# Kernel optimization log

Hardware: AMD Instinct MI355X
Metric: run time of the kernel (lower is better)

Reference implementation:

```python
import jax, jax.numpy as jnp
import numpy as np

N, M, E = 400000, 100000, 3200000
C_FEAT = 61            # per-point feature channels
D_IN = 64              # 3 (rel xyz) + C_FEAT
D0, D1, D2 = 64, 128, 256  # mlp = [64, 128, 256]
EPS = 1e-5


def setup_inputs() -> dict:
    key = jax.random.key(0)
    ks = jax.random.split(key, 16)
    inp = {}
    inp['point_bxyz'] = jax.random.uniform(ks[0], (N, 4), dtype=jnp.float32) * 50.0
    inp['point_feat'] = jax.random.normal(ks[1], (N, C_FEAT), dtype=jnp.float32)
    inp['sample_idx'] = jax.random.randint(ks[2], (M,), 0, N)
    inp['e_point'] = jax.random.randint(ks[3], (E,), 0, N)
    inp['e_new'] = jnp.sort(jax.random.randint(ks[4], (E,), 0, M))
    # PointConv: Linear(D_IN -> D0)
    inp['W0'] = jax.random.normal(ks[5], (D_IN, D0), dtype=jnp.float32) / np.sqrt(D_IN)
    inp['b0'] = jnp.zeros((D0,), dtype=jnp.float32)
    # mlp_convs[0]: Linear(D0 -> D1) + BN
    inp['W1'] = jax.random.normal(ks[6], (D0, D1), dtype=jnp.float32) / np.sqrt(D0)
    inp['b1'] = jnp.zeros((D1,), dtype=jnp.float32)
    inp['g1'] = jnp.ones((D1,), dtype=jnp.float32)
    inp['beta1'] = jnp.zeros((D1,), dtype=jnp.float32)
    # mlp_convs[1]: Linear(D1 -> D2) + BN
    inp['W2'] = jax.random.normal(ks[7], (D1, D2), dtype=jnp.float32) / np.sqrt(D1)
    inp['b2'] = jnp.zeros((D2,), dtype=jnp.float32)
    inp['g2'] = jnp.ones((D2,), dtype=jnp.float32)
    inp['beta2'] = jnp.zeros((D2,), dtype=jnp.float32)
    return inp


def _bn_relu(x, g, b):
    # BatchNorm1d in training mode: batch stats, biased variance
    mu = x.mean(axis=0)
    var = x.var(axis=0)
    return jax.nn.relu((x - mu) * jax.lax.rsqrt(var + EPS) * g + b)


def reference(point_bxyz, point_feat, sample_idx, e_point, e_new,
              W0, b0, W1, b1, g1, beta1, W2, b2, g2, beta2):
    num_new = sample_idx.shape[0]
    new_bxyz = point_bxyz[sample_idx]                      # [M, 4]
    # PointConv: per-edge relative position encoding + feature gather
    rel = point_bxyz[e_point, 1:4] - new_bxyz[e_new, 1:4]  # [E, 3]
    edge_in = jnp.concatenate([rel, point_feat[e_point]], axis=-1)  # [E, D_IN]
    h = jax.nn.relu(edge_in @ W0 + b0)                     # [E, D0]
    # per-neighborhood max aggregation (scatter-max), empty segments -> 0
    agg = jax.ops.segment_max(h, e_new, num_segments=num_new)
    agg = jnp.where(jnp.isneginf(agg), 0.0, agg)           # [M, D0]
    # trailing Linear + BN + ReLU stack
    x = _bn_relu(agg @ W1 + b1, g1, beta1)                 # [M, D1]
    x = _bn_relu(x @ W2 + b2, g2, beta2)                   # [M, D2]
    return new_bxyz, x
```

## Files before the change

### kernel.cpp

```cpp
#include <hip/hip_runtime.h>

#define EPS 1e-5f
#define ECHUNK 64
#define PF 8

typedef _Float16 half8 __attribute__((ext_vector_type(8)));
typedef _Float16 half4v __attribute__((ext_vector_type(4)));
typedef float float4v __attribute__((ext_vector_type(4)));

__global__ void gather_kernel(const float4* __restrict__ bxyz, const int* __restrict__ sidx,
                              float4* __restrict__ out, int M) {
    int i = blockIdx.x * blockDim.x + threadIdx.x;
    if (i < M) out[i] = bxyz[sidx[i]];
}

__global__ void w2t_kernel(const float* __restrict__ W2, _Float16* __restrict__ W2h) {
    int i = blockIdx.x * blockDim.x + threadIdx.x;
    int n = i & 255, k = i >> 8;
    W2h[(size_t)n * 128 + k] = (_Float16)W2[(size_t)k * 256 + n];
}

__global__ __launch_bounds__(256, 4) void point_kernel(
    const float* __restrict__ feat, const float4* __restrict__ bxyz4,
    const float* __restrict__ W0, const float* __restrict__ b0,
    _Float16* __restrict__ GDh, int N) {
    __shared__ float Xt[64 * 68];
    __shared__ float Ws[64 * 64];
    __shared__ float w0s[192];
    int t = threadIdx.x;
    int row0 = blockIdx.x * 64;
    for (int i = t; i < 64 * 61; i += 256) {
        int r = i / 61, k = i - r * 61;
        int rr = min(row0 + r, N - 1);
        Xt[k * 68 + r] = feat[(size_t)rr * 61 + k];
    }
    for (int i = t; i < 61 * 64; i += 256) {
        int k = i >> 6, c = i & 63;
        Ws[i] = W0[(size_t)(3 + k) * 64 + c];
    }
    if (t < 192) { int k = 61 + t / 64, j = t % 64; Xt[k * 68 + j] = 0.f; Ws[k * 64 + j] = 0.f; w0s[t] = W0[t]; }
    __syncthreads();
    int c0 = (t & 15) * 4;
    int r0 = (t >> 4) * 4;
    float acc[4][4] = {};
#pragma unroll 4
    for (int k = 0; k < 64; ++k) {
        float4 x = *(const float4*)&Xt[k * 68 + r0];
        float4 w = *(const float4*)&Ws[k * 64 + c0];
        float xv[4] = {x.x, x.y, x.z, x.w};
        float wv[4] = {w.x, w.y, w.z, w.w};
#pragma unroll
        for (int rr = 0; rr < 4; ++rr)
#pragma unroll
            for (int cc = 0; cc < 4; ++cc)
                acc[rr][cc] = fmaf(xv[rr], wv[cc], acc[rr][cc]);
    }
    float4 bb = *(const float4*)&b0[c0];
    float bv[4] = {bb.x, bb.y, bb.z, bb.w};
    float wx[4], wy[4], wz[4];
#pragma unroll
    for (int cc = 0; cc < 4; ++cc) {
        wx[cc] = w0s[c0 + cc];
        wy[cc] = w0s[64 + c0 + cc];
        wz[cc] = w0s[128 + c0 + cc];
    }
#pragma unroll
    for (int rr = 0; rr < 4; ++rr) {
        int r = row0 + r0 + rr;
        if (r < N) {
            float4 P = bxyz4[r];
            half4v o;
#pragma unroll
            for (int cc = 0; cc < 4; ++cc) {
                float d = fmaf(P.y, wx[cc], fmaf(P.z, wy[cc], P.w * wz[cc]));
                o[cc] = (_Float16)(acc[rr][cc] + bv[cc] + d);
            }
            *(half4v*)&GDh[(size_t)r * 64 + c0] = o;
        }
    }
}

__global__ __launch_bounds__(256, 4) void edge_kernel(
    const float4* __restrict__ nbxyz4,
    const int* __restrict__ e_point, const int* __restrict__ e_new,
    const _Float16* __restrict__ GDh, const float* __restrict__ W0,
    float* __restrict__ agg, int E) {
    int lane = threadIdx.x & 63;
    int gwave = blockIdx.x * 4 + (threadIdx.x >> 6);
    int base = gwave * ECHUNK;
    if (base >= E) return;
    int n = min(ECHUNK, E - base);
    int idx = min(base + lane, E - 1);
    int ep = e_point[idx];
    int en = e_new[idx];
    float wx = W0[lane], wy = W0[64 + lane], wz = W0[128 + lane];
    float runmax = 0.f;
    int curseg = -1;
    float S = 0.f;
    for (int g0 = 0; g0 < n; g0 += PF) {
        _Float16 gu[PF];
#pragma unroll
        for (int j = 0; j < PF; ++j) {
            int p = __builtin_amdgcn_readlane(ep, g0 + j);
            gu[j] = GDh[(size_t)p * 64 + lane];
        }
#pragma unroll
        for (int j = 0; j < PF; ++j) {
            if (g0 + j >= n) break;
            int s = __builtin_amdgcn_readlane(en, g0 + j);
            if (s != curseg) {
                if (curseg >= 0)
                    atomicMax((int*)&agg[(size_t)curseg * 64 + lane], __float_as_int(runmax));
                curseg = s;
                runmax = 0.f;
                float4 Q = nbxyz4[s];
                S = fmaf(Q.y, wx, fmaf(Q.z, wy, Q.w * wz));
            }
            float h = (float)gu[j] - S;
            runmax = fmaxf(runmax, h);
        }
    }
    if (curseg >= 0)
        atomicMax((int*)&agg[(size_t)curseg * 64 + lane], __float_as_int(runmax));
}

__global__ __launch_bounds__(256, 4) void gemm1_kernel(
    const float* __restrict__ agg, const float* __restrict__ W1,
    float* __restrict__ y1, float* __restrict__ p1sum, float* __restrict__ p1sq, int M) {
    __shared__ float Xt[64 * 68];
    __shared__ float Ws[64 * 128];
    float* red = Xt;
    int t = threadIdx.x;
    int row0 = blockIdx.x * 64;
#pragma unroll
    for (int j = 0; j < 4; ++j) {
        int idx4 = t + j * 256;
        int r = idx4 >> 4, k4 = idx4 & 15;
        float4 v = make_float4(0.f, 0.f, 0.f, 0.f);
        if (row0 + r < M) v = ((const float4*)agg)[(size_t)(row0 + r) * 16 + k4];
        Xt[(k4 * 4 + 0) * 68 + r] = v.x;
        Xt[(k4 * 4 + 1) * 68 + r] = v.y;
        Xt[(k4 * 4 + 2) * 68 + r] = v.z;
        Xt[(k4 * 4 + 3) * 68 + r] = v.w;
    }
#pragma unroll
    for (int j = 0; j < 8; ++j) {
        int idx4 = t + j * 256;
        ((float4*)Ws)[idx4] = ((const float4*)W1)[idx4];
    }
    __syncthreads();
    int c0 = (t & 15) * 8;
    int r0 = (t >> 4) * 4;
    float acc[4][8] = {};
#pragma unroll 4
    for (int k = 0; k < 64; ++k) {
        float4 x = *(const float4*)&Xt[k * 68 + r0];
        float4 wa = *(const float4*)&Ws[k * 128 + c0];
        float4 wb = *(const float4*)&Ws[k * 128 + c0 + 4];
        float xv[4] = {x.x, x.y, x.z, x.w};
        float wv[8] = {wa.x, wa.y, wa.z, wa.w, wb.x, wb.y, wb.z, wb.w};
#pragma unroll
        for (int rr = 0; rr < 4; ++rr)
#pragma unroll
            for (int cc = 0; cc < 8; ++cc)
                acc[rr][cc] = fmaf(xv[rr], wv[cc], acc[rr][cc]);
    }
    float s[8] = {}, q[8] = {};
#pragma unroll
    for (int rr = 0; rr < 4; ++rr) {
        int r = row0 + r0 + rr;
        if (r < M) {
            *(float4*)&y1[(size_t)r * 128 + c0] = make_float4(acc[rr][0], acc[rr][1], acc[rr][2], acc[rr][3]);
            *(float4*)&y1[(size_t)r * 128 + c0 + 4] = make_float4(acc[rr][4], acc[rr][5], acc[rr][6], acc[rr][7]);
        }
#pragma unroll
        for (int cc = 0; cc < 8; ++cc) { float a = acc[rr][cc]; s[cc] += a; q[cc] += a * a; }
    }
    __syncthreads();
    int colg = t & 15, rowg = t >> 4;
#pragma unroll
    for (int cc = 0; cc < 8; ++cc) {
        int c = colg * 8 + cc;
        red[c * 17 + rowg] = s[cc];
        red[2176 + c * 17 + rowg] = q[cc];
    }
    __syncthreads();
    if (t < 128) {
        float ss = 0.f, qq = 0.f;
#pragma unroll
        for (int i = 0; i < 16; ++i) { ss += red[t * 17 + i]; qq += red[2176 + t * 17 + i]; }
        p1sum[(size_t)blockIdx.x * 128 + t] = ss;
        p1sq[(size_t)blockIdx.x * 128 + t] = qq;
    }
}

__global__ void stats_kernel(const float* __restrict__ psum, const float* __restrict__ psq,
                             const float* __restrict__ g, const float* __restrict__ beta,
                             float* __restrict__ scale, float* __restrict__ shift,
                             int nblk, int ncols, float invM) {
    __shared__ float ss[256], qq[256];
    int c = blockIdx.x;
    int t = threadIdx.x;
    float s = 0.f, q = 0.f;
    for (int b = t; b < nblk; b += 256) {
        s += psum[(size_t)b * ncols + c];
        q += psq[(size_t)b * ncols + c];
    }
    ss[t] = s; qq[t] = q;
    __syncthreads();
    for (int off = 128; off > 0; off >>= 1) {
        if (t < off) { ss[t] += ss[t + off]; qq[t] += qq[t + off]; }
        __syncthreads();
    }
    if (t == 0) {
        float mean = ss[0] * invM;
        float var = qq[0] * invM - mean * mean;
        float sc = g[c] * rsqrtf(var + EPS);
        scale[c] = sc;
        shift[c] = beta[c] - mean * sc;
    }
}

__global__ __launch_bounds__(256, 2) void gemm2_kernel(
    const float* __restrict__ y1, const _Float16* __restrict__ W2h,
    const float* __restrict__ scale1, const float* __restrict__ shift1,
    float* __restrict__ yout, float* __restrict__ p2sum, float* __restrict__ p2sq,
    int M, int nbn) {
    __shared__ _Float16 As[128 * 136];
    __shared__ _Float16 Bs[128 * 136];
    int t = threadIdx.x;
    int bm = blockIdx.x / nbn;
    int bn = blockIdx.x % nbn;
    int row0 = bm * 128;
#pragma unroll
    for (int j = 0; j < 16; ++j) {
        int idx4 = t + j * 256;
        int r = idx4 >> 5, k4 = idx4 & 31;
        float4 v = make_float4(0.f, 0.f, 0.f, 0.f);
        if (row0 + r < M) {
            float4 y = ((const float4*)y1)[(size_t)(row0 + r) * 32 + k4];
            float4 sc = ((const float4*)scale1)[k4];
            float4 sh = ((const float4*)shift1)[k4];
            v.x = fmaxf(0.f, fmaf(y.x, sc.x, sh.x));
            v.y = fmaxf(0.f, fmaf(y.y, sc.y, sh.y));
            v.z = fmaxf(0.f, fmaf(y.z, sc.z, sh.z));
            v.w = fmaxf(0.f, fmaf(y.w, sc.w, sh.w));
        }
        half4v h;
        h[0] = (_Float16)v.x; h[1] = (_Float16)v.y; h[2] = (_Float16)v.z; h[3] = (_Float16)v.w;
        *(half4v*)&As[r * 136 + k4 * 4] = h;
    }
    int n0 = bn * 128;
#pragma unroll
    for (int j = 0; j < 8; ++j) {
        int idx8 = t + j * 256;
        int nn = idx8 >> 4, k8 = idx8 & 15;
        *(half8*)&Bs[nn * 136 + k8 * 8] = *(const half8*)&W2h[(size_t)(n0 + nn) * 128 + k8 * 8];
    }
    __syncthreads();
    int w = t >> 6, lane = t & 63;
    int quad = lane >> 4, l16 = lane & 15;
    int mwave = (w >> 1) * 64, nwave = (w & 1) * 64;
    float4v acc[4][4] = {};
#pragma unroll
    for (int kc = 0; kc < 4; ++kc) {
        int koff = kc * 32 + quad * 8;
        half8 af[4], bf[4];
#pragma unroll
        for (int mt = 0; mt < 4; ++mt)
            af[mt] = *(const half8*)&As[(mwave + mt * 16 + l16) * 136 + koff];
#pragma unroll
        for (int nt = 0; nt < 4; ++nt)
            bf[nt] = *(const half8*)&Bs[(nwave + nt * 16 + l16) * 136 + koff];
#pragma unroll
        for (int mt = 0; mt < 4; ++mt)
#pragma unroll
            for (int nt = 0; nt < 4; ++nt)
                acc[mt][nt] = __builtin_amdgcn_mfma_f32_16x16x32_f16(af[mt], bf[nt], acc[mt][nt], 0, 0, 0);
    }
    float s[4] = {}, q[4] = {};
    int colbase = n0 + nwave + l16;
#pragma unroll
    for (int mt = 0; mt < 4; ++mt) {
#pragma unroll
        for (int i = 0; i < 4; ++i) {
            int row = row0 + mwave + mt * 16 + quad * 4 + i;
            if (row < M) {
#pragma unroll
                for (int nt = 0; nt < 4; ++nt)
                    yout[(size_t)row * 256 + colbase + nt * 16] = acc[mt][nt][i];
            }
#pragma unroll
            for (int nt = 0; nt < 4; ++nt) {
                float a = acc[mt][nt][i];
                s[nt] += a; q[nt] += a * a;
            }
        }
    }
    __syncthreads();
    float* red = (float*)As;
    int slot = (w >> 1) * 4 + quad;
#pragma unroll
    for (int nt = 0; nt < 4; ++nt) {
        int c = (w & 1) * 64 + nt * 16 + l16;
        red[c * 8 + slot] = s[nt];
        red[1024 + c * 8 + slot] = q[nt];
    }
    __syncthreads();
    if (t < 128) {
        float ss = 0.f, qq = 0.f;
#pragma unroll
        for (int i = 0; i < 8; ++i) { ss += red[t * 8 + i]; qq += red[1024 + t * 8 + i]; }
        p2sum[(size_t)bm * 256 + n0 + t] = ss;
        p2sq[(size_t)bm * 256 + n0 + t] = qq;
    }
}

__global__ void apply2_kernel(float4* __restrict__ x, const float* __restrict__ scale2,
                              const float* __restrict__ shift2, int n4) {
    int i = blockIdx.x * blockDim.x + threadIdx.x;
    if (i >= n4) return;
    int c4 = i & 63;
    float4 v = x[i];
    float4 sc = ((const float4*)scale2)[c4];
    float4 sh = ((const float4*)shift2)[c4];
    v.x = fmaxf(0.f, fmaf(v.x, sc.x, sh.x));
    v.y = fmaxf(0.f, fmaf(v.y, sc.y, sh.y));
    v.z = fmaxf(0.f, fmaf(v.z, sc.z, sh.z));
    v.w = fmaxf(0.f, fmaf(v.w, sc.w, sh.w));
    x[i] = v;
}

extern "C" void kernel_launch(void* const* d_in, const int* in_sizes, int n_in,
                              void* d_out, int out_size, void* d_ws, size_t ws_size,
                              hipStream_t stream) {
    const float* bxyz  = (const float*)d_in[0];
    const float* feat  = (const float*)d_in[1];
    const int*   sidx  = (const int*)d_in[2];
    const int*   e_point = (const int*)d_in[3];
    const int*   e_new = (const int*)d_in[4];
    const float* W0    = (const float*)d_in[5];
    const float* b0    = (const float*)d_in[6];
    const float* W1    = (const float*)d_in[7];
    const float* g1    = (const float*)d_in[9];
    const float* beta1 = (const float*)d_in[10];
    const float* W2    = (const float*)d_in[11];
    const float* g2    = (const float*)d_in[13];
    const float* beta2 = (const float*)d_in[14];
    int N = in_sizes[0] / 4;
    int M = in_sizes[2];
    int E = in_sizes[3];

    float* out0 = (float*)d_out;
    float* out1 = (float*)d_out + (size_t)M * 4;

    float* ws = (float*)d_ws;
    size_t o = 0;
    float* agg = ws + o; o += (size_t)M * 64;
    float* y1  = ws + o; o += (size_t)M * 128;
    _Float16* GDh = (_Float16*)(ws + o); o += (size_t)N * 32;
    _Float16* W2h = (_Float16*)(ws + o); o += 128 * 256 / 2;
    int nblk1 = (M + 63) / 64;
    int nblk2m = (M + 127) / 128;
    int nbn = 2;
    float* p1sum = ws + o; o += (size_t)nblk1 * 128;
    float* p1sq  = ws + o; o += (size_t)nblk1 * 128;
    float* p2sum = ws + o; o += (size_t)nblk2m * 256;
    float* p2sq  = ws + o; o += (size_t)nblk2m * 256;
    float* scale1 = ws + o; o += 128;
    float* shift1 = ws + o; o += 128;
    float* scale2 = ws + o; o += 256;
    float* shift2 = ws + o; o += 256;

    hipMemsetAsync(agg, 0, (size_t)M * 64 * sizeof(float), stream);
    gather_kernel<<<(M + 255) / 256, 256, 0, stream>>>((const float4*)bxyz, sidx, (float4*)out0, M);
    w2t_kernel<<<128, 256, 0, stream>>>(W2, W2h);
    point_kernel<<<(N + 63) / 64, 256, 0, stream>>>(feat, (const float4*)bxyz, W0, b0, GDh, N);
    int nwaves = (E + ECHUNK - 1) / ECHUNK;
    edge_kernel<<<(nwaves + 3) / 4, 256, 0, stream>>>((const float4*)out0, e_point, e_new,
                                                      GDh, W0, agg, E);
    gemm1_kernel<<<nblk1, 256, 0, stream>>>(agg, W1, y1, p1sum, p1sq, M);
    stats_kernel<<<128, 256, 0, stream>>>(p1sum, p1sq, g1, beta1, scale1, shift1, nblk1, 128, 1.f / M);
    gemm2_kernel<<<nblk2m * nbn, 256, 0, stream>>>(y1, W2h, scale1, shift1, out1, p2sum, p2sq, M, nbn);
    stats_kernel<<<256, 256, 0, stream>>>(p2sum, p2sq, g2, beta2, scale2, shift2, nblk2m, 256, 1.f / M);
    apply2_kernel<<<((M * 64) + 255) / 256, 256, 0, stream>>>((float4*)out1, scale2, shift2, M * 64);
}
```

Baseline: 463.7 us.

## Move point and gemm1 GEMMs to fp16 MFMA and store y1 in fp16

Rewrites point_kernel and gemm1_kernel to use fp16 MFMA 16x16x32 instructions with 128-row tiles in place of scalar fp32 FMA loops. A single prep kernel now converts and transposes W0, W1 and W2 to fp16. The intermediate y1 is stored as fp16 to halve its traffic between gemm1 and gemm2. Point xyz is now folded into the GEMM input (fp16) rather than added in fp32, which lowers precision of the per-point features and the BN statistics inputs.

Result: faster. 404.8 us (-12.7%).

```diff
diff --git a/kernel.cpp b/kernel.cpp
--- a/kernel.cpp
+++ b/kernel.cpp
@@ -14,69 +14,93 @@
     if (i < M) out[i] = bxyz[sidx[i]];
 }
 
-__global__ void w2t_kernel(const float* __restrict__ W2, _Float16* __restrict__ W2h) {
+__global__ void prep_kernel(const float* __restrict__ W0, const float* __restrict__ W1,
+                            const float* __restrict__ W2, _Float16* __restrict__ W0t,
+                            _Float16* __restrict__ W1t, _Float16* __restrict__ W2t) {
     int i = blockIdx.x * blockDim.x + threadIdx.x;
-    int n = i & 255, k = i >> 8;
-    W2h[(size_t)n * 128 + k] = (_Float16)W2[(size_t)k * 256 + n];
+    if (i < 4096) {
+        int k = i >> 6, n = i & 63;
+        W0t[(size_t)n * 64 + k] = (_Float16)W0[i];
+    } else if (i < 12288) {
+        int j = i - 4096; int k = j >> 7, n = j & 127;
+        W1t[(size_t)n * 64 + k] = (_Float16)W1[j];
+    } else if (i < 45056) {
+        int j = i - 12288; int k = j >> 8, n = j & 255;
+        W2t[(size_t)n * 128 + k] = (_Float16)W2[j];
+    }
 }
 
 __global__ __launch_bounds__(256, 4) void point_kernel(
     const float* __restrict__ feat, const float4* __restrict__ bxyz4,
-    const float* __restrict__ W0, const float* __restrict__ b0,
+    const _Float16* __restrict__ W0t, const float* __restrict__ b0,
     _Float16* __restrict__ GDh, int N) {
-    __shared__ float Xt[64 * 68];
-    __shared__ float Ws[64 * 64];
-    __shared__ float w0s[192];
+    __shared__ _Float16 As[128 * 72];
     int t = threadIdx.x;
-    int row0 = blockIdx.x * 64;
-    for (int i = t; i < 64 * 61; i += 256) {
-        int r = i / 61, k = i - r * 61;
-        int rr = min(row0 + r, N - 1);
-        Xt[k * 68 + r] = feat[(size_t)rr * 61 + k];
-    }
-    for (int i = t; i < 61 * 64; i += 256) {
-        int k = i >> 6, c = i & 63;
-        Ws[i] = W0[(size_t)(3 + k) * 64 + c];
-    }
-    if (t < 192) { int k = 61 + t / 64, j = t % 64; Xt[k * 68 + j] = 0.f; Ws[k * 64 + j] = 0.f; w0s[t] = W0[t]; }
-    __syncthreads();
-    int c0 = (t & 15) * 4;
-    int r0 = (t >> 4) * 4;
-    float acc[4][4] = {};
-#pragma unroll 4
-    for (int k = 0; k < 64; ++k) {
-        float4 x = *(const float4*)&Xt[k * 68 + r0];
-        float4 w = *(const float4*)&Ws[k * 64 + c0];
-        float xv[4] = {x.x, x.y, x.z, x.w};
-        float wv[4] = {w.x, w.y, w.z, w.w};
-#pragma unroll
-        for (int rr = 0; rr < 4; ++rr)
-#pragma unroll
-            for (int cc = 0; cc < 4; ++cc)
-                acc[rr][cc] = fmaf(xv[rr], wv[cc], acc[rr][cc]);
-    }
-    float4 bb = *(const float4*)&b0[c0];
-    float bv[4] = {bb.x, bb.y, bb.z, bb.w};
-    float wx[4], wy[4], wz[4];
-#pragma unroll
-    for (int cc = 0; cc < 4; ++cc) {
-        wx[cc] = w0s[c0 + cc];
-        wy[cc] = w0s[64 + c0 + cc];
-        wz[cc] = w0s[128 + c0 + cc];
-    }
-#pragma unroll
-    for (int rr = 0; rr < 4; ++rr) {
-        int r = row0 + r0 + rr;
-        if (r < N) {
-            float4 P = bxyz4[r];
-            half4v o;
-#pragma unroll
-            for (int cc = 0; cc < 4; ++cc) {
-                float d = fmaf(P.y, wx[cc], fmaf(P.z, wy[cc], P.w * wz[cc]));
-                o[cc] = (_Float16)(acc[rr][cc] + bv[cc] + d);
-            }
-            *(half4v*)&GDh[(size_t)r * 64 + c0] = o;
-        }
+    int row0 = blockIdx.x * 128;
+    if (t < 128) {
+        int r = min(row0 + t, N - 1);
+        float4 P = bxyz4[r];
+        As[t * 72 + 0] = (_Float16)P.y;
+        As[t * 72 + 1] = (_Float16)P.z;
+        As[t * 72 + 2] = (_Float16)P.w;
+    }
+    const float* fbase = feat + (size_t)row0 * 61;
+    int avail = (int)min((size_t)7808, (size_t)(N - row0) * 61);
+#pragma unroll
+    for (int j = 0; j < 8; ++j) {
+        int base = (t + j * 256) * 4;
+        if (base < avail) {
+            float4 v = *(const float4*)&fbase[base];
+            float fv[4] = {v.x, v.y, v.z, v.w};
+#pragma unroll
+            for (int u = 0; u < 4; ++u) {
+                int flat = base + u;
+                int r = flat / 61;
+                int k = flat - r * 61;
+                As[r * 72 + 3 + k] = (_Float16)fv[u];
+            }
+        }
+    }
+    __syncthreads();
+    int w = t >> 6, lane = t & 63, quad = lane >> 4, l16 = lane & 15;
+    int mwave = w * 32;
+    float4v acc[2][4] = {};
+#pragma unroll
+    for (int kc = 0; kc < 2; ++kc) {
+        int koff = kc * 32 + quad * 8;
+        half8 af[2], bf[4];
+#pragma unroll
+        for (int mt = 0; mt < 2; ++mt)
+            af[mt] = *(const half8*)&As[(mwave + mt * 16 + l16) * 72 + koff];
+#pragma unroll
+        for (int nt = 0; nt < 4; ++nt)
+            bf[nt] = *(const half8*)&W0t[(size_t)(nt * 16 + l16) * 64 + koff];
+#pragma unroll
+        for (int mt = 0; mt < 2; ++mt)
+#pragma unroll
+            for (int nt = 0; nt < 4; ++nt)
+                acc[mt][nt] = __builtin_amdgcn_mfma_f32_16x16x32_f16(af[mt], bf[nt], acc[mt][nt], 0, 0, 0);
+    }
+    float b0v[4];
+#pragma unroll
+    for (int nt = 0; nt < 4; ++nt) b0v[nt] = b0[nt * 16 + l16];
+    __syncthreads();
+#pragma unroll
+    for (int mt = 0; mt < 2; ++mt)
+#pragma unroll
+        for (int i = 0; i < 4; ++i) {
+            int rloc = mwave + mt * 16 + quad * 4 + i;
+#pragma unroll
+            for (int nt = 0; nt < 4; ++nt)
+                As[rloc * 72 + nt * 16 + l16] = (_Float16)(acc[mt][nt][i] + b0v[nt]);
+        }
+    __syncthreads();
+#pragma unroll
+    for (int j = 0; j < 4; ++j) {
+        int i8 = t + j * 256;
+        int r = i8 >> 3, c8 = i8 & 7;
+        if (row0 + r < N)
+            *(half8*)&GDh[(size_t)(row0 + r) * 64 + c8 * 8] = *(const half8*)&As[r * 72 + c8 * 8];
     }
 }
 
@@ -124,73 +148,89 @@
         atomicMax((int*)&agg[(size_t)curseg * 64 + lane], __float_as_int(runmax));
 }
 
-__global__ __launch_bounds__(256, 4) void gemm1_kernel(
-    const float* __restrict__ agg, const float* __restrict__ W1,
-    float* __restrict__ y1, float* __restrict__ p1sum, float* __restrict__ p1sq, int M) {
-    __shared__ float Xt[64 * 68];
-    __shared__ float Ws[64 * 128];
-    float* red = Xt;
+__global__ __launch_bounds__(256, 2) void gemm1_kernel(
+    const float* __restrict__ agg, const _Float16* __restrict__ W1t,
+    _Float16* __restrict__ y1h, float* __restrict__ p1sum, float* __restrict__ p1sq, int M) {
+    __shared__ _Float16 As[128 * 72];
+    __shared__ float red[4096];
     int t = threadIdx.x;
-    int row0 = blockIdx.x * 64;
-#pragma unroll
-    for (int j = 0; j < 4; ++j) {
-        int idx4 = t + j * 256;
-        int r = idx4 >> 4, k4 = idx4 & 15;
+    int row0 = blockIdx.x * 128;
+#pragma unroll
+    for (int j = 0; j < 8; ++j) {
+        int i4 = t + j * 256;
+        int r = i4 >> 4, k4 = i4 & 15;
         float4 v = make_float4(0.f, 0.f, 0.f, 0.f);
         if (row0 + r < M) v = ((const float4*)agg)[(size_t)(row0 + r) * 16 + k4];
-        Xt[(k4 * 4 + 0) * 68 + r] = v.x;
-        Xt[(k4 * 4 + 1) * 68 + r] = v.y;
-        Xt[(k4 * 4 + 2) * 68 + r] = v.z;
-        Xt[(k4 * 4 + 3) * 68 + r] = v.w;
-    }
-#pragma unroll
-    for (int j = 0; j < 8; ++j) {
-        int idx4 = t + j * 256;
-        ((float4*)Ws)[idx4] = ((const float4*)W1)[idx4];
-    }
-    __syncthreads();
-    int c0 = (t & 15) * 8;
-    int r0 = (t >> 4) * 4;
-    float acc[4][8] = {};
-#pragma unroll 4
-    for (int k = 0; k < 64; ++k) {
-        float4 x = *(const float4*)&Xt[k * 68 + r0];
-        float4 wa = *(const float4*)&Ws[k * 128 + c0];
-        float4 wb = *(const float4*)&Ws[k * 128 + c0 + 4];
-        float xv[4] = {x.x, x.y, x.z, x.w};
-        float wv[8] = {wa.x, wa.y, wa.z, wa.w, wb.x, wb.y, wb.z, wb.w};
-#pragma unroll
-        for (int rr = 0; rr < 4; ++rr)
-#pragma unroll
-            for (int cc = 0; cc < 8; ++cc)
-                acc[rr][cc] = fmaf(xv[rr], wv[cc], acc[rr][cc]);
+        half4v h;
+        h[0] = (_Float16)v.x; h[1] = (_Float16)v.y; h[2] = (_Float16)v.z; h[3] = (_Float16)v.w;
+        *(half4v*)&As[r * 72 + k4 * 4] = h;
+    }
+    __syncthreads();
+    int w = t >> 6, lane = t & 63, quad = lane >> 4, l16 = lane & 15;
+    int mwave = w * 32;
+    float4v acc[2][8] = {};
+#pragma unroll
+    for (int kc = 0; kc < 2; ++kc) {
+        int koff = kc * 32 + quad * 8;
+        half8 af[2], bf[8];
+#pragma unroll
+        for (int mt = 0; mt < 2; ++mt)
+            af[mt] = *(const half8*)&As[(mwave + mt * 16 + l16) * 72 + koff];
+#pragma unroll
+        for (int nt = 0; nt < 8; ++nt)
+            bf[nt] = *(const half8*)&W1t[(size_t)(nt * 16 + l16) * 64 + koff];
+#pragma unroll
+        for (int mt = 0; mt < 2; ++mt)
+#pragma unroll
+            for (int nt = 0; nt < 8; ++nt)
+                acc[mt][nt] = __builtin_amdgcn_mfma_f32_16x16x32_f16(af[mt], bf[nt], acc[mt][nt], 0, 0, 0);
     }
     float s[8] = {}, q[8] = {};
 #pragma unroll
-    for (int rr = 0; rr < 4; ++rr) {
-        int r = row0 + r0 + rr;
-        if (r < M) {
-            *(float4*)&y1[(size_t)r * 128 + c0] = make_float4(acc[rr][0], acc[rr][1], acc[rr][2], acc[rr][3]);
-            *(float4*)&y1[(size_t)r * 128 + c0 + 4] = make_float4(acc[rr][4], acc[rr][5], acc[rr][6], acc[rr][7]);
-        }
-#pragma unroll
-        for (int cc = 0; cc < 8; ++cc) { float a = acc[rr][cc]; s[cc] += a; q[cc] += a * a; }
-    }
-    __syncthreads();
-    int colg = t & 15, rowg = t >> 4;
-#pragma unroll
-    for (int cc = 0; cc < 8; ++cc) {
-        int c = colg * 8 + cc;
-        red[c * 17 + rowg] = s[cc];
-        red[2176 + c * 17 + rowg] = q[cc];
+    for (int mt = 0; mt < 2; ++mt)
+#pragma unroll
+        for (int i = 0; i < 4; ++i)
+#pragma unroll
+            for (int nt = 0; nt < 8; ++nt) {
+                float a = acc[mt][nt][i];
+                s[nt] += a; q[nt] += a * a;
+            }
+    int slot = w * 4 + quad;
+#pragma unroll
+    for (int nt = 0; nt < 8; ++nt) {
+        int c = nt * 16 + l16;
+        red[c * 16 + slot] = s[nt];
+        red[2048 + c * 16 + slot] = q[nt];
     }
     __syncthreads();
     if (t < 128) {
         float ss = 0.f, qq = 0.f;
 #pragma unroll
-        for (int i = 0; i < 16; ++i) { ss += red[t * 17 + i]; qq += red[2176 + t * 17 + i]; }
+        for (int i = 0; i < 16; ++i) { ss += red[t * 16 + i]; qq += red[2048 + t * 16 + i]; }
         p1sum[(size_t)blockIdx.x * 128 + t] = ss;
         p1sq[(size_t)blockIdx.x * 128 + t] = qq;
+    }
+#pragma unroll
+    for (int half = 0; half < 2; ++half) {
+#pragma unroll
+        for (int mt = 0; mt < 2; ++mt)
+#pragma unroll
+            for (int i = 0; i < 4; ++i) {
+                int rloc = mwave + mt * 16 + quad * 4 + i;
+#pragma unroll
+                for (int nt = 0; nt < 4; ++nt)
+                    As[rloc * 72 + nt * 16 + l16] = (_Float16)acc[mt][half * 4 + nt][i];
+            }
+        __syncthreads();
+#pragma unroll
+        for (int j = 0; j < 4; ++j) {
+            int i8 = t + j * 256;
+            int r = i8 >> 3, c8 = i8 & 7;
+            if (row0 + r < M)
+                *(half8*)&y1h[(size_t)(row0 + r) * 128 + half * 64 + c8 * 8] =
+                    *(const half8*)&As[r * 72 + c8 * 8];
+        }
+        __syncthreads();
     }
 }
 
@@ -222,7 +262,7 @@
 }
 
 __global__ __launch_bounds__(256, 2) void gemm2_kernel(
-    const float* __restrict__ y1, const _Float16* __restrict__ W2h,
+    const _Float16* __restrict__ y1h, const _Float16* __restrict__ W2t,
     const float* __restrict__ scale1, const float* __restrict__ shift1,
     float* __restrict__ yout, float* __restrict__ p2sum, float* __restrict__ p2sq,
     int M, int nbn) {
@@ -233,29 +273,30 @@
     int bn = blockIdx.x % nbn;
     int row0 = bm * 128;
 #pragma unroll
-    for (int j = 0; j < 16; ++j) {
-        int idx4 = t + j * 256;
-        int r = idx4 >> 5, k4 = idx4 & 31;
-        float4 v = make_float4(0.f, 0.f, 0.f, 0.f);
+    for (int j = 0; j < 8; ++j) {
+        int i8 = t + j * 256;
+        int r = i8 >> 4, k8 = i8 & 15;
+        half8 hv = {};
         if (row0 + r < M) {
-            float4 y = ((const float4*)y1)[(size_t)(row0 + r) * 32 + k4];
-            float4 sc = ((const float4*)scale1)[k4];
-            float4 sh = ((const float4*)shift1)[k4];
-            v.x = fmaxf(0.f, fmaf(y.x, sc.x, sh.x));
-            v.y = fmaxf(0.f, fmaf(y.y, sc.y, sh.y));
-            v.z = fmaxf(0.f, fmaf(y.z, sc.z, sh.z));
-            v.w = fmaxf(0.f, fmaf(y.w, sc.w, sh.w));
-        }
-        half4v h;
-        h[0] = (_Float16)v.x; h[1] = (_Float16)v.y; h[2] = (_Float16)v.z; h[3] = (_Float16)v.w;
-        *(half4v*)&As[r * 136 + k4 * 4] = h;
+            half8 y = *(const half8*)&y1h[(size_t)(row0 + r) * 128 + k8 * 8];
+            float4 sca = ((const float4*)scale1)[k8 * 2];
+            float4 scb = ((const float4*)scale1)[k8 * 2 + 1];
+            float4 sha = ((const float4*)shift1)[k8 * 2];
+            float4 shb = ((const float4*)shift1)[k8 * 2 + 1];
+            float sc[8] = {sca.x, sca.y, sca.z, sca.w, scb.x, scb.y, scb.z, scb.w};
+            float sh[8] = {sha.x, sha.y, sha.z, sha.w, shb.x, shb.y, shb.z, shb.w};
+#pragma unroll
+            for (int u = 0; u < 8; ++u)
+                hv[u] = (_Float16)fmaxf(0.f, fmaf((float)y[u], sc[u], sh[u]));
+        }
+        *(half8*)&As[r * 136 + k8 * 8] = hv;
     }
     int n0 = bn * 128;
 #pragma unroll
     for (int j = 0; j < 8; ++j) {
-        int idx8 = t + j * 256;
-        int nn = idx8 >> 4, k8 = idx8 & 15;
-        *(half8*)&Bs[nn * 136 + k8 * 8] = *(const half8*)&W2h[(size_t)(n0 + nn) * 128 + k8 * 8];
+        int i8 = t + j * 256;
+        int nn = i8 >> 4, k8 = i8 & 15;
+        *(half8*)&Bs[nn * 136 + k8 * 8] = *(const half8*)&W2t[(size_t)(n0 + nn) * 128 + k8 * 8];
     }
     __syncthreads();
     int w = t >> 6, lane = t & 63;
@@ -357,10 +398,12 @@
     float* ws = (float*)d_ws;
     size_t o = 0;
     float* agg = ws + o; o += (size_t)M * 64;
-    float* y1  = ws + o; o += (size_t)M * 128;
+    _Float16* y1h = (_Float16*)(ws + o); o += (size_t)M * 64;
     _Float16* GDh = (_Float16*)(ws + o); o += (size_t)N * 32;
-    _Float16* W2h = (_Float16*)(ws + o); o += 128 * 256 / 2;
-    int nblk1 = (M + 63) / 64;
+    _Float16* W0t = (_Float16*)(ws + o); o += 2048;
+    _Float16* W1t = (_Float16*)(ws + o); o += 4096;
+    _Float16* W2t = (_Float16*)(ws + o); o += 16384;
+    int nblk1 = (M + 127) / 128;
     int nblk2m = (M + 127) / 128;
     int nbn = 2;
     float* p1sum = ws + o; o += (size_t)nblk1 * 128;
@@ -374,14 +417,14 @@
 
     hipMemsetAsync(agg, 0, (size_t)M * 64 * sizeof(float), stream);
     gather_kernel<<<(M + 255) / 256, 256, 0, stream>>>((const float4*)bxyz, sidx, (float4*)out0, M);
-    w2t_kernel<<<128, 256, 0, stream>>>(W2, W2h);
-    point_kernel<<<(N + 63) / 64, 256, 0, stream>>>(feat, (const float4*)bxyz, W0, b0, GDh, N);
+    prep_kernel<<<176, 256, 0, stream>>>(W0, W1, W2, W0t, W1t, W2t);
+    point_kernel<<<(N + 127) / 128, 256, 0, stream>>>(feat, (const float4*)bxyz, W0t, b0, GDh, N);
     int nwaves = (E + ECHUNK - 1) / ECHUNK;
     edge_kernel<<<(nwaves + 3) / 4, 256, 0, stream>>>((const float4*)out0, e_point, e_new,
                                                       GDh, W0, agg, E);
-    gemm1_kernel<<<nblk1, 256, 0, stream>>>(agg, W1, y1, p1sum, p1sq, M);
+    gemm1_kernel<<<nblk1, 256, 0, stream>>>(agg, W1t, y1h, p1sum, p1sq, M);
     stats_kernel<<<128, 256, 0, stream>>>(p1sum, p1sq, g1, beta1, scale1, shift1, nblk1, 128, 1.f / M);
-    gemm2_kernel<<<nblk2m * nbn, 256, 0, stream>>>(y1, W2h, scale1, shift1, out1, p2sum, p2sq, M, nbn);
+    gemm2_kernel<<<nblk2m * nbn, 256, 0, stream>>>(y1h, W2t, scale1, shift1, out1, p2sum, p2sq, M, nbn);
     stats_kernel<<<256, 256, 0, stream>>>(p2sum, p2sq, g2, beta2, scale2, shift2, nblk2m, 256, 1.f / M);
     apply2_kernel<<<((M * 64) + 255) / 256, 256, 0, stream>>>((float4*)out1, scale2, shift2, M * 64);
 }
```
